# Kernel tuning notes

Hardware: AMD Instinct MI355X
Metric: run time of the kernel (lower is better)

The kernel has to match this reference:

```python
import jax, jax.numpy as jnp
import numpy as np

NB_VEC = 4  # module init arg nbVec
TEMP = 20.0  # distance temperature in exp(-d/20)


def setup_inputs() -> dict:
    key = jax.random.key(0)
    k1, k2 = jax.random.split(key)
    B, C, H, W = 16, 64, 256, 256
    x = jax.random.normal(k1, (B, C, H, W), dtype=jnp.float32)
    # stands in for torch.rand score init used when prior is None
    score_init = jax.random.uniform(k2, (B, H * W), dtype=jnp.float32)
    return {"x": x, "score_init": score_init}


def reference(x, score_init):
    B, C, H, W = x.shape
    N = H * W
    # [B, N, C] flattened spatial features
    xf = jnp.transpose(x, (0, 2, 3, 1)).reshape(B, N, C)
    batch = jnp.arange(B)
    score = score_init
    vecs, sims = [], []
    for _ in range(NB_VEC):
        ind = jnp.argmax(score, axis=1)                      # [B] greedy pick
        raw = xf[batch, ind]                                 # [B, C]
        d2 = jnp.sum((xf - raw[:, None, :]) ** 2, axis=-1)   # [B, N]
        # safe sqrt (distance is exactly 0 at the selected pixel)
        sim = jnp.exp(-jnp.sqrt(jnp.maximum(d2, 1e-12)) / TEMP)
        simNorm = sim / jnp.sum(sim, axis=1, keepdims=True)
        reprVec = jnp.einsum('bnc,bn->bc', xf, simNorm)      # softmax-weighted agg
        vecs.append(reprVec)
        sims.append(sim.reshape(B, 1, H, W))
        score = (1.0 - sim) * score                          # suppress nearby pts
    vecList = jnp.stack(vecs, axis=1)                        # [B, nbVec, C]
    simList = jnp.concatenate(sims, axis=1)                  # [B, nbVec, H, W]
    # selectedPos is only incremented in the onlySimSample branch; zeros here
    selectedPos = jnp.zeros((B, 1, H, W), dtype=x.dtype)
    return vecList, simList, selectedPos
```

## Files before the change

### kernel.cpp

```cpp
#include <hip/hip_runtime.h>

#define BB 16
#define CC 64
#define NN 65536
#define NBV 4
#define B64 (BB * 64)


__global__ __launch_bounds__(256)
void k_argmax1(const float* __restrict__ sc_in,
               float* __restrict__ bval, int* __restrict__ bidx,
               float* __restrict__ sel_out) {
    int b = blockIdx.y, blk = blockIdx.x, tid = threadIdx.x;
    const float* s = sc_in + (size_t)b * NN + blk * 1024;
    float v = -1e30f; int vi = 0x7fffffff;
    #pragma unroll
    for (int k = 0; k < 4; k++) {
        int idx = k * 256 + tid;
        float xv = s[idx];
        if (xv > v) { v = xv; vi = blk * 1024 + idx; }
    }
    size_t gt = ((size_t)(b * 64 + blk)) * 256 + tid;
    #pragma unroll
    for (int k = 0; k < 4; k++) sel_out[gt + (size_t)k * 262144] = 0.f;
    __shared__ float sv[256]; __shared__ int si[256];
    sv[tid] = v; si[tid] = vi;
    __syncthreads();
    for (int st = 128; st > 0; st >>= 1) {
        if (tid < st) {
            float ov = sv[tid + st]; int oi = si[tid + st];
            if (ov > sv[tid] || (ov == sv[tid] && oi < si[tid])) { sv[tid] = ov; si[tid] = oi; }
        }
        __syncthreads();
    }
    if (tid == 0) { bval[b * 64 + blk] = sv[0]; bidx[b * 64 + blk] = si[0]; }
}

__global__ __launch_bounds__(256, 2)
void k_iter(const float* __restrict__ x, const float* __restrict__ score_in,
            float* __restrict__ score_out,
            float* __restrict__ bval, int* __restrict__ bidx,
            float* __restrict__ wpart, float* __restrict__ sspart,
            float* __restrict__ sim_out, int iter) {
    int b = blockIdx.y, blk = blockIdx.x, tid = threadIdx.x;
    int lane = tid & 63, wv = tid >> 6;
    __shared__ float raw_s[64];
    __shared__ float4 d2p[2][4][64];

    int rb = (iter & 1) * B64, wb = ((iter & 1) ^ 1) * B64;

    if (tid < 64) {
        float v = bval[rb + b * 64 + tid]; int vi = bidx[rb + b * 64 + tid];
        #pragma unroll
        for (int off = 32; off >= 1; off >>= 1) {
            float ov = __shfl_down(v, off, 64); int oi = __shfl_down(vi, off, 64);
            if (ov > v || (ov == v && oi < vi)) { v = ov; vi = oi; }
        }
        int ind = __shfl(vi, 0, 64);
        raw_s[tid] = x[((size_t)b * 64 + tid) * NN + ind];
    }
    __syncthreads();

    const float* xb = x + ((size_t)b * 64 + wv * 16) * NN;
    float raw[16];
    #pragma unroll
    for (int j = 0; j < 16; j++) raw[j] = raw_s[wv * 16 + j];
    float acc[16];
    #pragma unroll
    for (int j = 0; j < 16; j++) acc[j] = 0.f;

    const size_t sb = (size_t)b * NN;
    const size_t simb = (size_t)(b * NBV + iter) * NN;
    const bool w0 = (wv == 0), upd = (iter < 3);

    float ssacc = 0.f, smax = -1e30f; int smaxi = 0;
    float4 sc_next;
    if (w0 && upd) sc_next = *(const float4*)(score_in + sb + blk * 1024 + lane * 4);

    #pragma unroll 1
    for (int g = 0; g < 4; g++) {
        int n0 = blk * 1024 + g * 256 + lane * 4;
        float4 xv[16];
        #pragma unroll
        for (int j = 0; j < 16; j++) xv[j] = *(const float4*)(xb + (size_t)j * NN + n0);
        float4 sc_cur = sc_next;
        if (w0 && upd && g < 3) sc_next = *(const float4*)(score_in + sb + n0 + 256);
        float4 d2 = make_float4(0.f, 0.f, 0.f, 0.f);
        #pragma unroll
        for (int j = 0; j < 16; j++) {
            float r = raw[j];
            float dx = xv[j].x - r, dy = xv[j].y - r, dz = xv[j].z - r, dw = xv[j].w - r;
            d2.x = fmaf(dx, dx, d2.x); d2.y = fmaf(dy, dy, d2.y);
            d2.z = fmaf(dz, dz, d2.z); d2.w = fmaf(dw, dw, d2.w);
        }
        d2p[g & 1][wv][lane] = d2;
        __syncthreads();
        float4 a0 = d2p[g & 1][0][lane], a1 = d2p[g & 1][1][lane];
        float4 a2 = d2p[g & 1][2][lane], a3 = d2p[g & 1][3][lane];
        float4 sim;
        sim.x = expf(-sqrtf(fmaxf((a0.x + a1.x) + (a2.x + a3.x), 1e-12f)) * 0.05f);
        sim.y = expf(-sqrtf(fmaxf((a0.y + a1.y) + (a2.y + a3.y), 1e-12f)) * 0.05f);
        sim.z = expf(-sqrtf(fmaxf((a0.z + a1.z) + (a2.z + a3.z), 1e-12f)) * 0.05f);
        sim.w = expf(-sqrtf(fmaxf((a0.w + a1.w) + (a2.w + a3.w), 1e-12f)) * 0.05f);
        #pragma unroll
        for (int j = 0; j < 16; j++) {
            acc[j] = fmaf(sim.x, xv[j].x, acc[j]);
            acc[j] = fmaf(sim.y, xv[j].y, acc[j]);
            acc[j] = fmaf(sim.z, xv[j].z, acc[j]);
            acc[j] = fmaf(sim.w, xv[j].w, acc[j]);
        }
        if (w0) {
            ssacc += (sim.x + sim.y) + (sim.z + sim.w);
            *(float4*)(sim_out + simb + n0) = sim;
            if (upd) {
                float4 sc;
                sc.x = sc_cur.x * (1.f - sim.x);
                sc.y = sc_cur.y * (1.f - sim.y);
                sc.z = sc_cur.z * (1.f - sim.z);
                sc.w = sc_cur.w * (1.f - sim.w);
                *(float4*)(score_out + sb + n0) = sc;
                if (sc.x > smax) { smax = sc.x; smaxi = n0; }
                if (sc.y > smax) { smax = sc.y; smaxi = n0 + 1; }
                if (sc.z > smax) { smax = sc.z; smaxi = n0 + 2; }
                if (sc.w > smax) { smax = sc.w; smaxi = n0 + 3; }
            }
        }
    }

    #pragma unroll
    for (int j = 0; j < 16; j++) {
        float v = acc[j];
        #pragma unroll
        for (int off = 32; off >= 1; off >>= 1) v += __shfl_down(v, off, 64);
        if (lane == 0) wpart[(((size_t)b * 64) + blk) * 64 + wv * 16 + j] = v;
    }
    if (w0) {
        float v = ssacc;
        #pragma unroll
        for (int off = 32; off >= 1; off >>= 1) v += __shfl_down(v, off, 64);
        if (lane == 0) sspart[b * 64 + blk] = v;
        if (upd) {
            #pragma unroll
            for (int off = 32; off >= 1; off >>= 1) {
                float ov = __shfl_down(smax, off, 64); int oi = __shfl_down(smaxi, off, 64);
                if (ov > smax || (ov == smax && oi < smaxi)) { smax = ov; smaxi = oi; }
            }
            if (lane == 0) { bval[wb + b * 64 + blk] = smax; bidx[wb + b * 64 + blk] = smaxi; }
        }
    }
}

__global__ void k_fin(const float* __restrict__ wpart, const float* __restrict__ sspart,
                      float* __restrict__ vec_out, int iter) {
    int b = blockIdx.x, tid = threadIdx.x;
    float w = 0.f;
    for (int blk = 0; blk < 64; blk++) w += wpart[(((size_t)b * 64) + blk) * 64 + tid];
    float ss = 0.f;
    for (int blk = 0; blk < 64; blk++) ss += sspart[b * 64 + blk];
    vec_out[(b * NBV + iter) * 64 + tid] = w / ss;
}

extern "C" void kernel_launch(void* const* d_in, const int* in_sizes, int n_in,
                              void* d_out, int out_size, void* d_ws, size_t ws_size,
                              hipStream_t stream) {
    const float* x = (const float*)d_in[0];
    const float* sc_in = (const float*)d_in[1];
    float* out = (float*)d_out;
    float* vec_out = out;
    float* sim_out = vec_out + (size_t)BB * NBV * CC;
    float* sel_out = sim_out + (size_t)BB * NBV * NN;

    float* ws = (float*)d_ws;
    float* score = ws;
    float* bval = ws + (size_t)BB * NN;
    int* bidx = (int*)(bval + 2 * B64);
    float* wpart = bval + 4 * B64;
    float* sspart = wpart + (size_t)BB * 64 * 64;

    k_argmax1<<<dim3(64, BB), 256, 0, stream>>>(sc_in, bval, bidx, sel_out);
    for (int it = 0; it < NBV; it++) {
        const float* s_in = (it == 0) ? sc_in : score;
        k_iter<<<dim3(64, BB), 256, 0, stream>>>(x, s_in, score, bval, bidx,
                                                 wpart, sspart, sim_out, it);
        k_fin<<<dim3(BB), 64, 0, stream>>>(wpart, sspart, vec_out, it);
    }
}
```

Before: 546.1 us.

## Pre-transpose x into pixel-blocked channel tiles for contiguous per-block reads

Adds a kernel that rewrites x into a blocked layout, grouped by block of 256 pixels and then by channel, stored in workspace. Each iteration kernel then reads each group's 64 channels from one contiguous 64KB region instead of 64 rows spaced by the plane stride. The aim is better DRAM page and TLB locality across the four passes over x. In exchange it adds a full extra read and write of x (512MB of traffic) and needs a much larger workspace. The per-wave loads were already coalesced in 1KB runs, so the gain may not cover the extra pass.

```diff
diff --git a/kernel.cpp b/kernel.cpp
--- a/kernel.cpp
+++ b/kernel.cpp
@@ -36,9 +36,23 @@
     if (tid == 0) { bval[b * 64 + blk] = sv[0]; bidx[b * 64 + blk] = si[0]; }
 }
 
+__global__ __launch_bounds__(256)
+void k_xpose(const float* __restrict__ x, float* __restrict__ xT) {
+    int b = blockIdx.y;
+    int c = blockIdx.x >> 4, seg = blockIdx.x & 15;
+    int tid = threadIdx.x, lane = tid & 63, wv = tid >> 6;
+    const float* rp = x + ((size_t)b * 64 + c) * NN + seg * 4096;
+    #pragma unroll
+    for (int i = 0; i < 4; i++) {
+        float4 v = *(const float4*)(rp + i * 1024 + tid * 4);
+        int gg = seg * 16 + i * 4 + wv;
+        *(float4*)(xT + (((size_t)b * 256 + gg) * 64 + c) * 256 + lane * 4) = v;
+    }
+}
+
 __global__ __launch_bounds__(256, 2)
-void k_iter(const float* __restrict__ x, const float* __restrict__ score_in,
-            float* __restrict__ score_out,
+void k_iter(const float* __restrict__ xT, const float* __restrict__ x,
+            const float* __restrict__ score_in, float* __restrict__ score_out,
             float* __restrict__ bval, int* __restrict__ bidx,
             float* __restrict__ wpart, float* __restrict__ sspart,
             float* __restrict__ sim_out, int iter) {
@@ -61,7 +75,7 @@
     }
     __syncthreads();
 
-    const float* xb = x + ((size_t)b * 64 + wv * 16) * NN;
+    const float* xtb = xT + (((size_t)b * 256 + blk * 4) * 64 + wv * 16) * 256;
     float raw[16];
     #pragma unroll
     for (int j = 0; j < 16; j++) raw[j] = raw_s[wv * 16 + j];
@@ -80,9 +94,10 @@
     #pragma unroll 1
     for (int g = 0; g < 4; g++) {
         int n0 = blk * 1024 + g * 256 + lane * 4;
+        const float* tp = xtb + (size_t)g * 64 * 256;
         float4 xv[16];
         #pragma unroll
-        for (int j = 0; j < 16; j++) xv[j] = *(const float4*)(xb + (size_t)j * NN + n0);
+        for (int j = 0; j < 16; j++) xv[j] = *(const float4*)(tp + j * 256 + lane * 4);
         float4 sc_cur = sc_next;
         if (w0 && upd && g < 3) sc_next = *(const float4*)(score_in + sb + n0 + 256);
         float4 d2 = make_float4(0.f, 0.f, 0.f, 0.f);
@@ -171,16 +186,18 @@
     float* sel_out = sim_out + (size_t)BB * NBV * NN;
 
     float* ws = (float*)d_ws;
-    float* score = ws;
-    float* bval = ws + (size_t)BB * NN;
+    float* xT = ws;
+    float* score = xT + (size_t)BB * NN * CC;
+    float* bval = score + (size_t)BB * NN;
     int* bidx = (int*)(bval + 2 * B64);
     float* wpart = bval + 4 * B64;
     float* sspart = wpart + (size_t)BB * 64 * 64;
 
     k_argmax1<<<dim3(64, BB), 256, 0, stream>>>(sc_in, bval, bidx, sel_out);
+    k_xpose<<<dim3(1024, BB), 256, 0, stream>>>(x, xT);
     for (int it = 0; it < NBV; it++) {
         const float* s_in = (it == 0) ? sc_in : score;
-        k_iter<<<dim3(64, BB), 256, 0, stream>>>(x, s_in, score, bval, bidx,
+        k_iter<<<dim3(64, BB), 256, 0, stream>>>(xT, x, s_in, score, bval, bidx,
                                                  wpart, sspart, sim_out, it);
         k_fin<<<dim3(BB), 64, 0, stream>>>(wpart, sspart, vec_out, it);
     }
```

New measurement: 623.6 us. 14.2% more time.
